# Kernel optimization log

Hardware: AMD Instinct MI355X
Metric: run time of the kernel (lower is better)

Reference implementation:

```python
import jax, jax.numpy as jnp
import numpy as np

K = 20
EPS = 1e-5


def _lrelu(x):
    return jax.nn.leaky_relu(x, 0.2)


def _bn(x, axes):
    # Training-mode batch norm with default affine (gamma=1, beta=0)
    m = jnp.mean(x, axis=axes, keepdims=True)
    v = jnp.var(x, axis=axes, keepdims=True)
    return (x - m) / jnp.sqrt(v + EPS)


def _get_graph_feature(x, k):
    # x: [B, C, N] -> [B, 2C, N, k]
    xx = jnp.sum(x * x, axis=1)                     # [B, N]
    inner = jnp.einsum('bcn,bcm->bnm', x, x)        # [B, N, N]
    pd = 2.0 * inner - xx[:, :, None] - xx[:, None, :]  # -||xi-xj||^2
    idx = jax.lax.top_k(pd, k)[1]                   # [B, N, k] nearest neighbors
    xt = jnp.transpose(x, (0, 2, 1))                # [B, N, C]
    feat = jax.vmap(lambda a, i: a[i])(xt, idx)     # [B, N, k, C] gathered neighbors
    center = jnp.broadcast_to(xt[:, :, None, :], feat.shape)
    out = jnp.concatenate([feat - center, center], axis=-1)  # [B, N, k, 2C]
    return jnp.transpose(out, (0, 3, 1, 2))


def _pconv(w, x):
    # 1x1 Conv2d, no bias: [O,C] x [B,C,N,k] -> [B,O,N,k]
    return jnp.einsum('oc,bcnk->bonk', w, x)


def _transform_net(x0, t_w1, t_w2, t_w3, t_fc1_w, t_fc2_w, t_fc2_b, t_fc3_w, t_fc3_b):
    h = _lrelu(_bn(_pconv(t_w1, x0), (0, 2, 3)))    # [B,64,N,k]
    h = _lrelu(_bn(_pconv(t_w2, h), (0, 2, 3)))     # [B,128,N,k]
    h = jnp.max(h, axis=-1)                         # [B,128,N]
    h = jnp.einsum('oc,bcn->bon', t_w3, h)          # [B,1024,N]
    h = _lrelu(_bn(h, (0, 2)))
    h = jnp.max(h, axis=-1)                         # [B,1024]
    h = _lrelu(_bn(h @ t_fc1_w.T, (0,)))            # [B,512]
    h = _lrelu(_bn(h @ t_fc2_w.T + t_fc2_b, (0,)))  # [B,256]
    h = h @ t_fc3_w.T + t_fc3_b                     # [B,9]
    h = h + jnp.eye(3, dtype=h.dtype).reshape(1, 9)
    return h.reshape(-1, 3, 3)


def setup_inputs() -> dict:
    key = jax.random.key(0)
    ks = jax.random.split(key, 16)
    s = 0.05
    B, N = 8, 1024
    return {
        'x': jax.random.normal(ks[0], (B, 3, N), jnp.float32),
        't_w1': jax.random.normal(ks[1], (64, 6), jnp.float32) * s,
        't_w2': jax.random.normal(ks[2], (128, 64), jnp.float32) * s,
        't_w3': jax.random.normal(ks[3], (1024, 128), jnp.float32) * s,
        't_fc1_w': jax.random.normal(ks[4], (512, 1024), jnp.float32) * s,
        't_fc2_w': jax.random.normal(ks[5], (256, 512), jnp.float32) * s,
        't_fc2_b': jnp.zeros((256,), jnp.float32),
        't_fc3_w': jax.random.normal(ks[6], (9, 256), jnp.float32) * s,
        't_fc3_b': jnp.zeros((9,), jnp.float32),
        'w1': jax.random.normal(ks[7], (64, 6), jnp.float32) * s,
        'w2': jax.random.normal(ks[8], (64, 128), jnp.float32) * s,
        'w3': jax.random.normal(ks[9], (128, 128), jnp.float32) * s,
        'w4': jax.random.normal(ks[10], (256, 256), jnp.float32) * s,
        'w6': jax.random.normal(ks[11], (1024, 512), jnp.float32) * s,
    }


def reference(x, t_w1, t_w2, t_w3, t_fc1_w, t_fc2_w, t_fc2_b, t_fc3_w, t_fc3_b,
              w1, w2, w3, w4, w6):
    # Input transform
    x0 = _get_graph_feature(x, K)                   # [B,6,N,k]
    T = _transform_net(x0, t_w1, t_w2, t_w3, t_fc1_w, t_fc2_w, t_fc2_b,
                       t_fc3_w, t_fc3_b)            # [B,3,3]
    x = jnp.einsum('bij,bjn->bin', T, x)            # [B,3,N]

    # EdgeConv stack
    g = _get_graph_feature(x, K)
    x1 = jnp.max(_lrelu(_bn(_pconv(w1, g), (0, 2, 3))), axis=-1)   # [B,64,N]
    g = _get_graph_feature(x1, K)
    x2 = jnp.max(_lrelu(_bn(_pconv(w2, g), (0, 2, 3))), axis=-1)   # [B,64,N]
    g = _get_graph_feature(x2, K)
    x3 = jnp.max(_lrelu(_bn(_pconv(w3, g), (0, 2, 3))), axis=-1)   # [B,128,N]
    g = _get_graph_feature(x3, K)
    x4 = jnp.max(_lrelu(_bn(_pconv(w4, g), (0, 2, 3))), axis=-1)   # [B,256,N]

    x_cat = jnp.concatenate([x1, x2, x3, x4], axis=1)              # [B,512,N]
    x_fea = x_cat  # adapt_layer_off: source unavailable, identity passthrough

    h = jnp.einsum('oc,bcn->bon', w6, x_fea)                       # [B,1024,N]
    h = _lrelu(_bn(h, (0, 2)))
    return jnp.max(h, axis=-1)                                     # [B,1024]
```

## Files before the change

kernel.cpp:

```cpp
#include <hip/hip_runtime.h>
#include <math.h>

#define BN_ 8
#define NN 1024
#define KK 20
#define EPSBN 1e-5f
#define FXSCALE 1048576.0f

typedef unsigned long long u64;

__device__ __forceinline__ float lrelu(float x){ return x > 0.f ? x : 0.2f*x; }

__device__ __forceinline__ unsigned fmap(float x){
  unsigned u = __float_as_uint(x);
  return (u & 0x80000000u) ? ~u : (u | 0x80000000u);
}
__device__ __forceinline__ float funmap(unsigned m){
  unsigned u = (m & 0x80000000u) ? (m & 0x7FFFFFFFu) : ~m;
  return __uint_as_float(u);
}

__device__ __forceinline__ int mbcnt64(u64 m){
  return __builtin_amdgcn_mbcnt_hi((unsigned)(m >> 32),
         __builtin_amdgcn_mbcnt_lo((unsigned)m, 0));
}

__device__ __forceinline__ void statadd(u64* SP, int O, int ch, int o, float s, float s2){
  atomicAdd(&SP[(size_t)ch*2*O + o],     (u64)(long long)llrintf(s  * FXSCALE));
  atomicAdd(&SP[(size_t)ch*2*O + O + o], (u64)(long long)llrintf(s2 * FXSCALE));
}

__global__ void k_transq(const float* __restrict__ src, long bs, int C,
                         float* __restrict__ xt, float* __restrict__ xx)
{
  int g = blockIdx.x*256 + threadIdx.x;
  if (g >= BN_*NN) return;
  int b = g >> 10, n = g & 1023;
  const float* s = src + (long)b*bs + n;
  float* d = xt + (long)g*C;
  float ss = 0.f;
  for (int c = 0; c < C; ++c){ float v = s[(long)c*NN]; d[c] = v; ss += v*v; }
  xx[g] = ss;
}

__global__ __launch_bounds__(256) void k_knn(
    const float* __restrict__ X, long bsX,
    const float* __restrict__ XT, const float* __restrict__ XX,
    int* __restrict__ IDX, int C)
{
  extern __shared__ float sm[];
  int tid = threadIdx.x;
  int wave = tid >> 6, lane = tid & 63;
  int b = blockIdx.x >> 7;
  int i0 = (blockIdx.x & 127) << 3;
  for (int t = tid; t < 8*C; t += 256){
    int rr = t / C, cc = t - rr*C;
    sm[t] = XT[((long)(b<<10) + i0 + rr)*C + cc];
  }
  __syncthreads();
  const float* xb = X + (long)b*bsX;
  float acc[2][16];
  #pragma unroll
  for (int r=0;r<2;r++)
    #pragma unroll
    for (int q=0;q<16;q++) acc[r][q]=0.f;
  const float* xi = sm + (wave*2)*C;
  for (int c = 0; c < C; ++c){
    const float4* xr4 = (const float4*)(xb + (long)c*NN);
    float4 xv4[4];
    #pragma unroll
    for (int q4=0;q4<4;q4++) xv4[q4] = xr4[q4*64 + lane];
    #pragma unroll
    for (int r=0;r<2;r++){
      float xiv = xi[r*C + c];
      #pragma unroll
      for (int q4=0;q4<4;q4++){
        acc[r][q4*4+0] = fmaf(xiv, xv4[q4].x, acc[r][q4*4+0]);
        acc[r][q4*4+1] = fmaf(xiv, xv4[q4].y, acc[r][q4*4+1]);
        acc[r][q4*4+2] = fmaf(xiv, xv4[q4].z, acc[r][q4*4+2]);
        acc[r][q4*4+3] = fmaf(xiv, xv4[q4].w, acc[r][q4*4+3]);
      }
    }
  }
  const float4* xx4 = (const float4*)(XX + (b<<10));
  float xxj[16];
  #pragma unroll
  for (int q4=0;q4<4;q4++){
    float4 t = xx4[q4*64 + lane];
    xxj[q4*4+0]=t.x; xxj[q4*4+1]=t.y; xxj[q4*4+2]=t.z; xxj[q4*4+3]=t.w;
  }
  const float* xxb = XX + (b<<10);
  int row0 = i0 + wave*2;
  #pragma unroll
  for (int r=0;r<2;r++){
    float xxi = xxb[row0 + r];
    #pragma unroll
    for (int q=0;q<16;q++) acc[r][q] = 2.f*acc[r][q] - xxi - xxj[q];
  }

  for (int r=0;r<2;r++){
    unsigned u[16];
    #pragma unroll
    for (int q=0;q<16;q++) u[q] = fmap(acc[r][q]);
    unsigned P = 0;
    for (int bit = 31; bit >= 0; --bit){
      unsigned cand = P | (1u << bit);
      int c = 0;
      #pragma unroll
      for (int q=0;q<16;q++) c += (int)__popcll(__ballot(u[q] >= cand));
      if (c >= KK) P = cand;
    }
    int nG = 0;
    #pragma unroll
    for (int q=0;q<16;q++) nG += (int)__popcll(__ballot(u[q] > P));
    int navail = KK - nG;
    int slot = 0;
    int outb = ((b<<10) + row0 + r)*KK;
    #pragma unroll
    for (int q=0;q<16;q++){
      u64 mg = __ballot(u[q] > P);
      u64 me = __ballot(u[q] == P);
      int cg = (int)__popcll(mg);
      int ce = (int)__popcll(me);
      int take_e = navail < ce ? navail : ce;
      int nval = ((q >> 2) << 8) + (lane << 2) + (q & 3);
      if (u[q] > P){
        IDX[outb + slot + mbcnt64(mg)] = nval;
      } else if (u[q] == P){
        int rk = mbcnt64(me);
        if (rk < take_e) IDX[outb + slot + cg + rk] = nval;
      }
      slot += cg + take_e;
      navail -= take_e;
    }
  }
}

__global__ void k_edgeconv3(const float* __restrict__ XT, const int* __restrict__ IDX,
                            const float* __restrict__ W, float* __restrict__ YMT,
                            u64* __restrict__ SP)
{
  __shared__ float nb[KK*3];
  __shared__ float ctr[3];
  __shared__ int is[KK];
  const int C = 3, O = 64;
  int tid = threadIdx.x;
  int bn = blockIdx.x;
  int b = bn >> 10;
  if (tid < KK) is[tid] = IDX[bn*KK + tid];
  __syncthreads();
  if (tid < 60){ int k = tid/3, c = tid - k*3; nb[tid] = XT[((long)(b<<10)+is[k])*C + c]; }
  if (tid < 3) ctr[tid] = XT[(long)bn*C + tid];
  __syncthreads();
  int o = tid;
  const float* wp = W + (long)o*2*C;
  float yc = 0.f;
  #pragma unroll
  for (int c = 0; c < 3; ++c) yc = fmaf(wp[C+c] - wp[c], ctr[c], yc);
  float acc[KK];
  #pragma unroll
  for (int k=0;k<KK;k++) acc[k] = yc;
  #pragma unroll
  for (int c = 0; c < 3; ++c){
    float wf = wp[c];
    #pragma unroll
    for (int k=0;k<KK;k++) acc[k] = fmaf(wf, nb[k*3+c], acc[k]);
  }
  float mx = -INFINITY, s = 0.f, s2 = 0.f;
  #pragma unroll
  for (int k=0;k<KK;k++){ float v = acc[k]; mx = fmaxf(mx, v); s += v; s2 = fmaf(v,v,s2); }
  YMT[(long)bn*O + o] = mx;
  statadd(SP, O, bn & 63, o, s, s2);
}

template<int C, int O>
__global__ __launch_bounds__(256) void k_gemm_ab(
    const float* __restrict__ XT, const float* __restrict__ WP,
    float* __restrict__ AB)
{
  constexpr int P = 16;
  constexpr int TWO = 2*O;
  constexpr int CO = (TWO + 255)/256;
  __shared__ __align__(16) float Xs[P][C];
  int tid = threadIdx.x;
  long bn0 = (long)blockIdx.x * P;
  for (int t = tid; t < P*C; t += 256) (&Xs[0][0])[t] = XT[bn0*C + t];
  __syncthreads();
  float acc[CO][P];
  #pragma unroll
  for (int j=0;j<CO;j++)
    #pragma unroll
    for (int r=0;r<P;r++) acc[j][r] = 0.f;
  for (int c4 = 0; c4 < C/4; ++c4){
    float4 w[CO];
    #pragma unroll
    for (int j=0;j<CO;j++){
      int o = tid + j*256;
      if (o < TWO) w[j] = *(const float4*)(WP + ((size_t)c4*TWO + o)*4);
    }
    #pragma unroll
    for (int r=0;r<P;r++){
      float4 xv = *(const float4*)(&Xs[r][c4*4]);
      #pragma unroll
      for (int j=0;j<CO;j++){
        acc[j][r] = fmaf(w[j].x, xv.x, acc[j][r]);
        acc[j][r] = fmaf(w[j].y, xv.y, acc[j][r]);
        acc[j][r] = fmaf(w[j].z, xv.z, acc[j][r]);
        acc[j][r] = fmaf(w[j].w, xv.w, acc[j][r]);
      }
    }
  }
  #pragma unroll
  for (int j=0;j<CO;j++){
    int o = tid + j*256;
    if (o < TWO)
      for (int r=0;r<P;r++) AB[(bn0 + r)*TWO + o] = acc[j][r];
  }
}

template<int O, int P>
__global__ __launch_bounds__(256) void k_egather(
    const float* __restrict__ AB, const int* __restrict__ IDX,
    float* __restrict__ YMT, u64* __restrict__ SP)
{
  constexpr int TWO = 2*O;
  constexpr int S = 256/O;
  constexpr int PS = P/S;
  __shared__ int is[P][KK];
  int tid = threadIdx.x;
  long bn0 = (long)blockIdx.x * P;
  long b10 = (bn0 >> 10) << 10;
  for (int t = tid; t < P*KK; t += 256) (&is[0][0])[t] = IDX[bn0*KK + t];
  __syncthreads();
  int strand = tid / O;
  int o = tid - strand*O;
  float s = 0.f, s2 = 0.f;
  #pragma unroll
  for (int ps = 0; ps < PS; ++ps){
    int p = strand*PS + ps;
    long bn = bn0 + p;
    float bv = AB[bn*TWO + O + o];
    float mx = -INFINITY;
    #pragma unroll
    for (int k = 0; k < KK; ++k){
      long row = b10 + is[p][k];
      float v = AB[row*TWO + o] + bv;
      mx = fmaxf(mx, v);
      s += v; s2 = fmaf(v,v,s2);
    }
    YMT[bn*O + o] = mx;
  }
  int ch = ((int)blockIdx.x * S + strand) & 63;
  statadd(SP, O, ch, o, s, s2);
}

__global__ void k_bnfin(const u64* __restrict__ SP, float* __restrict__ MV, int O, float cnt)
{
  int o = blockIdx.x*blockDim.x + threadIdx.x;
  if (o >= O) return;
  long long S = 0, S2 = 0;
  for (int ch = 0; ch < 64; ++ch){
    S  += (long long)SP[(size_t)ch*2*O + o];
    S2 += (long long)SP[(size_t)ch*2*O + O + o];
  }
  double m = (double)S / ((double)FXSCALE * (double)cnt);
  double ms2 = (double)S2 / ((double)FXSCALE * (double)cnt);
  double var = ms2 - m*m;
  MV[o] = (float)m;
  MV[O + o] = (float)(1.0 / sqrt(var + (double)EPSBN));
}

__global__ __launch_bounds__(64) void k_tconv2(
    const float* __restrict__ XT, const int* __restrict__ IDX,
    const float* __restrict__ W1, const float* __restrict__ MV1,
    const float* __restrict__ W2T, float* __restrict__ M2T, u64* __restrict__ SP)
{
  __shared__ float nb[KK*3];
  __shared__ float ctr[3];
  __shared__ __align__(16) float h1t[64*KK];
  __shared__ int is[KK];
  int tid = threadIdx.x;
  int bn = blockIdx.x;
  int b = bn >> 10;
  if (tid < KK) is[tid] = IDX[bn*KK + tid];
  __syncthreads();
  if (tid < 60){ int k = tid/3, c = tid - k*3; nb[tid] = XT[((long)(b<<10)+is[k])*3 + c]; }
  if (tid < 3) ctr[tid] = XT[(long)bn*3 + tid];
  __syncthreads();
  {
    const float* wp = W1 + tid*6;
    float w0=wp[0], w1=wp[1], w2=wp[2];
    float cterm = fmaf(wp[3]-w0, ctr[0], fmaf(wp[4]-w1, ctr[1], (wp[5]-w2)*ctr[2]));
    float m = MV1[tid], iv = MV1[64+tid];
    #pragma unroll
    for (int k=0;k<KK;k++){
      float y = cterm;
      y = fmaf(w0, nb[k*3],   y);
      y = fmaf(w1, nb[k*3+1], y);
      y = fmaf(w2, nb[k*3+2], y);
      h1t[tid*KK + k] = lrelu((y - m) * iv);
    }
  }
  __syncthreads();
  float acc[2][KK];
  #pragma unroll
  for (int j=0;j<2;j++)
    #pragma unroll
    for (int k=0;k<KK;k++) acc[j][k]=0.f;
  #pragma unroll 2
  for (int c=0;c<64;++c){
    float wv0 = W2T[c*128 + tid];
    float wv1 = W2T[c*128 + 64 + tid];
    const float4* hp = (const float4*)(h1t + c*KK);
    float hv[KK];
    #pragma unroll
    for (int q=0;q<5;q++){
      float4 v4 = hp[q];
      hv[q*4]=v4.x; hv[q*4+1]=v4.y; hv[q*4+2]=v4.z; hv[q*4+3]=v4.w;
    }
    #pragma unroll
    for (int k=0;k<KK;k++){
      acc[0][k] = fmaf(wv0, hv[k], acc[0][k]);
      acc[1][k] = fmaf(wv1, hv[k], acc[1][k]);
    }
  }
  int ch = bn & 63;
  #pragma unroll
  for (int j=0;j<2;j++){
    int o = tid + j*64;
    float mx=-INFINITY, s=0.f, s2=0.f;
    #pragma unroll
    for (int k=0;k<KK;k++){ float v = acc[j][k]; mx = fmaxf(mx, v); s += v; s2 = fmaf(v,v,s2); }
    M2T[(long)bn*128 + o] = mx;
    statadd(SP, 128, ch, o, s, s2);
  }
}

__global__ void k_apply_t(const float* __restrict__ SRC, const float* __restrict__ MV,
                          int O, float* __restrict__ DST, long dbs, int choff,
                          float* __restrict__ XTN, float* __restrict__ XXN)
{
  int bn = blockIdx.x*64 + threadIdx.x;
  if (bn >= BN_*NN) return;
  int b = bn >> 10, n = bn & 1023;
  const float4* src = (const float4*)(SRC + (long)bn*O);
  float4* xo = XTN ? (float4*)(XTN + (long)bn*O) : nullptr;
  float ss = 0.f;
  for (int o4 = 0; o4 < O/4; ++o4){
    float4 v = src[o4];
    float vv[4] = {v.x, v.y, v.z, v.w};
    float rr[4];
    #pragma unroll
    for (int u=0;u<4;u++){
      int o = o4*4+u;
      float t = lrelu((vv[u] - MV[o]) * MV[O+o]);
      rr[u] = t;
      ss = fmaf(t,t,ss);
      DST[(long)b*dbs + (long)(choff+o)*NN + n] = t;
    }
    if (xo) xo[o4] = make_float4(rr[0],rr[1],rr[2],rr[3]);
  }
  if (XXN) XXN[bn] = ss;
}

__global__ void k_wprep_t(const float* __restrict__ W, float* __restrict__ WT, int O, int C)
{
  int g = blockIdx.x*256+threadIdx.x;
  if (g >= O*C) return;
  int o = g / C, c = g - o*C;
  WT[(long)c*O + o] = W[g];
}

__global__ void k_wprep_q(const float* __restrict__ W, float* __restrict__ WQ, int C)
{
  int g = blockIdx.x*256+threadIdx.x;
  if (g >= 1024*C) return;
  int o = g / C, c = g - o*C;
  int j = o >> 8, t = o & 255;
  WQ[((size_t)c*256 + t)*4 + j] = W[g];
}

__global__ void k_wprep_e2(const float* __restrict__ W, float* __restrict__ WP, int O, int C)
{
  int g = blockIdx.x*256+threadIdx.x;
  if (g >= O*C) return;
  int o = g / C, c = g - o*C;
  float wf = W[(long)o*2*C + c];
  float wc = W[(long)o*2*C + C + c];
  size_t base = ((size_t)(c>>2)*(2*O))*4 + (c&3);
  WP[base + (size_t)o*4]       = wf;
  WP[base + (size_t)(O+o)*4]   = wc - wf;
}

__global__ __launch_bounds__(256, 1) void k_gemm_sm(
    const float* __restrict__ WQ, const float* __restrict__ X,
    long bsX, int C, unsigned* __restrict__ MX, u64* __restrict__ SP)
{
  int tid = threadIdx.x;
  int bt = blockIdx.x;
  int b = bt >> 6;
  int n0 = (bt & 63) << 4;
  const float* xrow = X + (long)b*bsX + n0;
  float acc[4][16];
  #pragma unroll
  for (int j=0;j<4;j++)
    #pragma unroll
    for (int i=0;i<16;i++) acc[j][i]=0.f;
  const float4* wq = (const float4*)WQ;

  auto loadX = [&](int cc, float4* dst){
    const float4* xc = (const float4*)(xrow + (size_t)cc*NN);
    dst[0]=xc[0]; dst[1]=xc[1]; dst[2]=xc[2]; dst[3]=xc[3];
  };
  auto gemm_step = [&](const float4* xq, float4 wv){
    float4 xa = xq[0], xb2 = xq[1], xe = xq[2], xf = xq[3];
    float wj[4] = {wv.x, wv.y, wv.z, wv.w};
    #pragma unroll
    for (int j=0;j<4;j++){
      float ww = wj[j];
      acc[j][0]=fmaf(ww,xa.x,acc[j][0]);  acc[j][1]=fmaf(ww,xa.y,acc[j][1]);
      acc[j][2]=fmaf(ww,xa.z,acc[j][2]);  acc[j][3]=fmaf(ww,xa.w,acc[j][3]);
      acc[j][4]=fmaf(ww,xb2.x,acc[j][4]);  acc[j][5]=fmaf(ww,xb2.y,acc[j][5]);
      acc[j][6]=fmaf(ww,xb2.z,acc[j][6]);  acc[j][7]=fmaf(ww,xb2.w,acc[j][7]);
      acc[j][8]=fmaf(ww,xe.x,acc[j][8]);  acc[j][9]=fmaf(ww,xe.y,acc[j][9]);
      acc[j][10]=fmaf(ww,xe.z,acc[j][10]); acc[j][11]=fmaf(ww,xe.w,acc[j][11]);
      acc[j][12]=fmaf(ww,xf.x,acc[j][12]); acc[j][13]=fmaf(ww,xf.y,acc[j][13]);
      acc[j][14]=fmaf(ww,xf.z,acc[j][14]); acc[j][15]=fmaf(ww,xf.w,acc[j][15]);
    }
  };

  float4 xc0[4], xc1[4], xn0[4], xn1[4];
  loadX(0, xc0); loadX(1, xc1);
  float4 w0 = wq[tid];
  float4 w1 = wq[256 + tid];
  for (int c = 0; c < C-2; c += 2){
    loadX(c+2, xn0); loadX(c+3, xn1);
    float4 p0 = wq[(size_t)(c+2)*256 + tid];
    float4 p1 = wq[(size_t)(c+3)*256 + tid];
    gemm_step(xc0, w0);
    gemm_step(xc1, w1);
    #pragma unroll
    for (int i=0;i<4;i++){ xc0[i]=xn0[i]; xc1[i]=xn1[i]; }
    w0 = p0; w1 = p1;
  }
  gemm_step(xc0, w0);
  gemm_step(xc1, w1);

  int ch = bt & 63;
  #pragma unroll
  for (int j=0;j<4;j++){
    int o = tid + j*256;
    float mx=-INFINITY, s=0.f, s2=0.f;
    #pragma unroll
    for (int i=0;i<16;i++){ float v=acc[j][i]; mx=fmaxf(mx,v); s+=v; s2=fmaf(v,v,s2); }
    atomicMax(&MX[(b<<10) + o], fmap(mx));
    statadd(SP, 1024, ch, o, s, s2);
  }
}

__global__ void k_finmax(const unsigned* __restrict__ MX, const float* __restrict__ MV,
                         float* __restrict__ OUT)
{
  int g = blockIdx.x*256+threadIdx.x;
  if (g >= BN_*1024) return;
  int o = g & 1023;
  OUT[g] = lrelu((funmap(MX[g]) - MV[o]) * MV[1024+o]);
}

__global__ __launch_bounds__(256) void k_fcbn(
    const float* __restrict__ A, const float* __restrict__ W,
    const float* __restrict__ bias, int C, int F, float* __restrict__ Z)
{
  int wv = threadIdx.x >> 6, lane = threadIdx.x & 63;
  int f = blockIdx.x*4 + wv;
  if (f >= F) return;
  const float* w = W + (long)f*C;
  float acc[8];
  #pragma unroll
  for (int b=0;b<8;b++) acc[b]=0.f;
  for (int c = lane; c < C; c += 64){
    float wvv = w[c];
    #pragma unroll
    for (int b=0;b<8;b++) acc[b] = fmaf(wvv, A[b*C + c], acc[b]);
  }
  #pragma unroll
  for (int b=0;b<8;b++){
    #pragma unroll
    for (int off=32; off>0; off>>=1) acc[b] += __shfl_xor(acc[b], off);
  }
  float bs = bias ? bias[f] : 0.f;
  float m = 0.f;
  #pragma unroll
  for (int b=0;b<8;b++){ acc[b] += bs; m += acc[b]; }
  m *= 0.125f;
  float var = 0.f;
  #pragma unroll
  for (int b=0;b<8;b++){ float d = acc[b]-m; var = fmaf(d,d,var); }
  var *= 0.125f;
  float is = rsqrtf(var + EPSBN);
  if (lane < 8) Z[lane*F + f] = lrelu((acc[lane]-m)*is);
}

__global__ __launch_bounds__(256) void k_fc3w(
    const float* __restrict__ A, const float* __restrict__ W,
    const float* __restrict__ bias, float* __restrict__ T9)
{
  int g = blockIdx.x*4 + (threadIdx.x >> 6);
  int lane = threadIdx.x & 63;
  if (g >= 72) return;
  int b = g / 9, j = g - b*9;
  const float* a = A + b*256;
  const float* w = W + j*256;
  float s = 0.f;
  for (int c = lane; c < 256; c += 64) s = fmaf(a[c], w[c], s);
  #pragma unroll
  for (int off=32; off>0; off>>=1) s += __shfl_xor(s, off);
  if (lane == 0){
    s += bias[j];
    if (j==0 || j==4 || j==8) s += 1.f;
    T9[g] = s;
  }
}

__global__ void k_tapply(const float* __restrict__ Xin, const float* __restrict__ T9,
                         float* __restrict__ Xtr)
{
  int g = blockIdx.x*256+threadIdx.x;
  if (g >= BN_*3*NN) return;
  int n = g & 1023;
  int i = (g >> 10) % 3;
  int b = g / (3*NN);
  const float* t = T9 + b*9 + i*3;
  const float* xb = Xin + (long)b*3*NN + n;
  Xtr[g] = fmaf(t[0], xb[0], fmaf(t[1], xb[NN], t[2]*xb[2*NN]));
}

extern "C" void kernel_launch(void* const* d_in, const int* in_sizes, int n_in,
                              void* d_out, int out_size, void* d_ws, size_t ws_size,
                              hipStream_t stream)
{
  (void)in_sizes; (void)n_in; (void)out_size;
  const float* x     = (const float*)d_in[0];
  const float* tw1   = (const float*)d_in[1];
  const float* tw2   = (const float*)d_in[2];
  const float* tw3   = (const float*)d_in[3];
  const float* tfc1w = (const float*)d_in[4];
  const float* tfc2w = (const float*)d_in[5];
  const float* tfc2b = (const float*)d_in[6];
  const float* tfc3w = (const float*)d_in[7];
  const float* tfc3b = (const float*)d_in[8];
  const float* w1    = (const float*)d_in[9];
  const float* w2    = (const float*)d_in[10];
  const float* w3    = (const float*)d_in[11];
  const float* w4    = (const float*)d_in[12];
  const float* w6    = (const float*)d_in[13];
  float* out = (float*)d_out;

  char* ws = (char*)d_ws;
  size_t off = 0;
  auto alloc = [&](size_t bytes) -> void* {
    off = (off + 255) & ~(size_t)255;
    void* p = ws + off;
    off += bytes;
    return p;
  };
  auto spb = [](int O){ return (size_t)64*2*O*8; };

  float*    xt   = (float*)alloc((size_t)BN_*NN*128*4);
  float*    xx   = (float*)alloc((size_t)BN_*NN*4);
  int*      idx  = (int*)  alloc((size_t)BN_*NN*KK*4);
  float*    ymt  = (float*)alloc((size_t)BN_*NN*256*4);
  float*    ab   = (float*)alloc((size_t)BN_*NN*512*4);
  float*    xcat = (float*)alloc((size_t)BN_*512*NN*4);
  float*    xtr  = (float*)alloc((size_t)BN_*3*NN*4);
  float*    m2   = (float*)alloc((size_t)BN_*128*NN*4);
  size_t zoff0 = (off + 255) & ~(size_t)255;
  u64*      sp_e1 = (u64*)alloc(spb(64));
  u64*      sp_tc = (u64*)alloc(spb(128));
  u64*      sp_g1 = (u64*)alloc(spb(1024));
  u64*      sp_L1 = (u64*)alloc(spb(64));
  u64*      sp_L2 = (u64*)alloc(spb(64));
  u64*      sp_L3 = (u64*)alloc(spb(128));
  u64*      sp_L4 = (u64*)alloc(spb(256));
  u64*      sp_g2 = (u64*)alloc(spb(1024));
  unsigned* mxu1  = (unsigned*)alloc((size_t)BN_*1024*4);
  unsigned* mxu2  = (unsigned*)alloc((size_t)BN_*1024*4);
  size_t ztotal = off - zoff0;
  float*    mv1  = (float*)alloc(2*64*4);
  float*    mv2  = (float*)alloc(2*128*4);
  float*    mv3  = (float*)alloc(2*1024*4);
  float*    mvL  = (float*)alloc(2*256*4);
  float*    mv6  = (float*)alloc(2*1024*4);
  float*    vbuf = (float*)alloc((size_t)BN_*1024*4);
  float*    z1   = (float*)alloc((size_t)BN_*512*4);
  float*    z2   = (float*)alloc((size_t)BN_*256*4);
  float*    T9   = (float*)alloc(72*4);
  float*    wt3q = (float*)alloc((size_t)128*1024*4);
  float*    w6q  = (float*)alloc((size_t)512*1024*4);
  float*    wt2t = (float*)alloc((size_t)64*128*4);
  float*    w2p  = (float*)alloc((size_t)64*128*4);
  float*    w3p  = (float*)alloc((size_t)64*256*4);
  float*    w4p  = (float*)alloc((size_t)128*512*4);
  if (off > ws_size) return;

  float* m2t = ymt;

  const float CNTK = 8.f*1024.f*20.f;
  const float CNTN = 8.f*1024.f;

  hipMemsetAsync((char*)ws + zoff0, 0, ztotal, stream);

  k_wprep_t<<<(128*64+255)/256, 256, 0, stream>>>(tw2, wt2t, 128, 64);
  k_wprep_q<<<(1024*128)/256, 256, 0, stream>>>(tw3, wt3q, 128);
  k_wprep_q<<<(1024*512)/256, 256, 0, stream>>>(w6, w6q, 512);
  k_wprep_e2<<<(64*64+255)/256, 256, 0, stream>>>(w2, w2p, 64, 64);
  k_wprep_e2<<<(128*64+255)/256, 256, 0, stream>>>(w3, w3p, 128, 64);
  k_wprep_e2<<<(256*128+255)/256, 256, 0, stream>>>(w4, w4p, 256, 128);

  k_transq<<<32, 256, 0, stream>>>(x, 3L*NN, 3, xt, xx);
  k_knn<<<1024, 256, 8*3*4, stream>>>(x, 3L*NN, xt, xx, idx, 3);
  k_edgeconv3<<<BN_*NN, 64, 0, stream>>>(xt, idx, tw1, ymt, sp_e1);
  k_bnfin<<<1, 64, 0, stream>>>(sp_e1, mv1, 64, CNTK);
  k_tconv2<<<BN_*NN, 64, 0, stream>>>(xt, idx, tw1, mv1, wt2t, m2t, sp_tc);
  k_bnfin<<<2, 64, 0, stream>>>(sp_tc, mv2, 128, CNTK);
  k_apply_t<<<128, 64, 0, stream>>>(m2t, mv2, 128, m2, 128L*NN, 0, nullptr, nullptr);
  k_gemm_sm<<<BN_*64, 256, 0, stream>>>(wt3q, m2, 128L*NN, 128, mxu1, sp_g1);
  k_bnfin<<<16, 64, 0, stream>>>(sp_g1, mv3, 1024, CNTN);
  k_finmax<<<32, 256, 0, stream>>>(mxu1, mv3, vbuf);
  k_fcbn<<<128, 256, 0, stream>>>(vbuf, tfc1w, nullptr, 1024, 512, z1);
  k_fcbn<<<64, 256, 0, stream>>>(z1, tfc2w, tfc2b, 512, 256, z2);
  k_fc3w<<<18, 256, 0, stream>>>(z2, tfc3w, tfc3b, T9);
  k_tapply<<<(BN_*3*NN)/256, 256, 0, stream>>>(x, T9, xtr);

  k_transq<<<32, 256, 0, stream>>>(xtr, 3L*NN, 3, xt, xx);
  k_knn<<<1024, 256, 8*3*4, stream>>>(xtr, 3L*NN, xt, xx, idx, 3);
  k_edgeconv3<<<BN_*NN, 64, 0, stream>>>(xt, idx, w1, ymt, sp_L1);
  k_bnfin<<<1, 64, 0, stream>>>(sp_L1, mvL, 64, CNTK);
  k_apply_t<<<128, 64, 0, stream>>>(ymt, mvL, 64, xcat, 512L*NN, 0, xt, xx);
  k_knn<<<1024, 256, 8*64*4, stream>>>(xcat, 512L*NN, xt, xx, idx, 64);
  k_gemm_ab<64,64><<<512, 256, 0, stream>>>(xt, w2p, ab);
  k_egather<64,16><<<512, 256, 0, stream>>>(ab, idx, ymt, sp_L2);
  k_bnfin<<<1, 64, 0, stream>>>(sp_L2, mvL, 64, CNTK);
  k_apply_t<<<128, 64, 0, stream>>>(ymt, mvL, 64, xcat, 512L*NN, 64, xt, xx);
  k_knn<<<1024, 256, 8*64*4, stream>>>(xcat + 64L*NN, 512L*NN, xt, xx, idx, 64);
  k_gemm_ab<64,128><<<512, 256, 0, stream>>>(xt, w3p, ab);
  k_egather<128,16><<<512, 256, 0, stream>>>(ab, idx, ymt, sp_L3);
  k_bnfin<<<2, 64, 0, stream>>>(sp_L3, mvL, 128, CNTK);
  k_apply_t<<<128, 64, 0, stream>>>(ymt, mvL, 128, xcat, 512L*NN, 128, xt, xx);
  k_knn<<<1024, 256, 8*128*4, stream>>>(xcat + 128L*NN, 512L*NN, xt, xx, idx, 128);
  k_gemm_ab<128,256><<<512, 256, 0, stream>>>(xt, w4p, ab);
  k_egather<256,16><<<512, 256, 0, stream>>>(ab, idx, ymt, sp_L4);
  k_bnfin<<<4, 64, 0, stream>>>(sp_L4, mvL, 256, CNTK);
  k_apply_t<<<128, 64, 0, stream>>>(ymt, mvL, 256, xcat, 512L*NN, 256, nullptr, nullptr);

  k_gemm_sm<<<BN_*64, 256, 0, stream>>>(w6q, xcat, 512L*NN, 512, mxu2, sp_g2);
  k_bnfin<<<16, 64, 0, stream>>>(sp_g2, mv6, 1024, CNTN);
  k_finmax<<<32, 256, 0, stream>>>(mxu2, mv6, out);
}
```

Measured before the change: 861.4 us.

## Run final 512→1024 conv GEMM on bf16 MFMA with fused max/BN stats

Replaces the fp32 SIMT GEMM for the final w6 layer with a bf16 MFMA 16x16x32 kernel. The weights are pre-swizzled into fragment layout, and k_apply_t additionally writes a bf16 point-major copy of the concatenated features via LDS staging. The goal is to cut the FMA-bound cost of the largest GEMM, at the price of bf16 rounding in the BN statistics and max, plus extra writes in apply. The k_gemm_sm prefetch double-buffer is also simplified, which affects the transform-net GEMM.

```diff
diff --git a/kernel.cpp b/kernel.cpp
--- a/kernel.cpp
+++ b/kernel.cpp
@@ -8,6 +8,9 @@
 #define FXSCALE 1048576.0f
 
 typedef unsigned long long u64;
+typedef unsigned short ushort_t;
+typedef __attribute__((ext_vector_type(8))) short short8v;
+typedef __attribute__((ext_vector_type(4))) float f32x4;
 
 __device__ __forceinline__ float lrelu(float x){ return x > 0.f ? x : 0.2f*x; }
 
@@ -18,6 +21,11 @@
 __device__ __forceinline__ float funmap(unsigned m){
   unsigned u = (m & 0x80000000u) ? (m & 0x7FFFFFFFu) : ~m;
   return __uint_as_float(u);
+}
+__device__ __forceinline__ ushort_t f2b(float f){
+  unsigned u = __float_as_uint(f);
+  unsigned r = (u + 0x7FFFu + ((u >> 16) & 1u)) >> 16;
+  return (ushort_t)r;
 }
 
 __device__ __forceinline__ int mbcnt64(u64 m){
@@ -338,10 +346,11 @@
 
 __global__ void k_apply_t(const float* __restrict__ SRC, const float* __restrict__ MV,
                           int O, float* __restrict__ DST, long dbs, int choff,
-                          float* __restrict__ XTN, float* __restrict__ XXN)
-{
+                          float* __restrict__ XTN, float* __restrict__ XXN,
+                          ushort_t* __restrict__ XB)
+{
+  extern __shared__ ushort_t lb[];
   int bn = blockIdx.x*64 + threadIdx.x;
-  if (bn >= BN_*NN) return;
   int b = bn >> 10, n = bn & 1023;
   const float4* src = (const float4*)(SRC + (long)bn*O);
   float4* xo = XTN ? (float4*)(XTN + (long)bn*O) : nullptr;
@@ -357,10 +366,19 @@
       rr[u] = t;
       ss = fmaf(t,t,ss);
       DST[(long)b*dbs + (long)(choff+o)*NN + n] = t;
+      if (XB) lb[threadIdx.x*O + o] = f2b(t);
     }
     if (xo) xo[o4] = make_float4(rr[0],rr[1],rr[2],rr[3]);
   }
   if (XXN) XXN[bn] = ss;
+  if (XB){
+    __syncthreads();
+    long bn0 = (long)blockIdx.x*64;
+    for (int r = 0; r < 64; ++r){
+      for (int t2 = threadIdx.x; t2 < O; t2 += 64)
+        XB[(bn0 + r)*512 + choff + t2] = lb[r*O + t2];
+    }
+  }
 }
 
 __global__ void k_wprep_t(const float* __restrict__ W, float* __restrict__ WT, int O, int C)
@@ -378,6 +396,17 @@
   int o = g / C, c = g - o*C;
   int j = o >> 8, t = o & 255;
   WQ[((size_t)c*256 + t)*4 + j] = W[g];
+}
+
+__global__ void k_wprep_mf(const float* __restrict__ W, ushort_t* __restrict__ WB)
+{
+  int g = blockIdx.x*256+threadIdx.x;
+  if (g >= 1024*512) return;
+  int o = g >> 9, c = g & 511;
+  int ks = c >> 5, kk = c & 31;
+  int l = (kk >> 3)*16 + (o & 15);
+  int e = kk & 7;
+  WB[(((size_t)(o >> 4)*16 + ks)*64 + l)*8 + e] = f2b(W[g]);
 }
 
 __global__ void k_wprep_e2(const float* __restrict__ W, float* __restrict__ WP, int O, int C)
@@ -408,12 +437,9 @@
     for (int i=0;i<16;i++) acc[j][i]=0.f;
   const float4* wq = (const float4*)WQ;
 
-  auto loadX = [&](int cc, float4* dst){
+  auto gemm_step = [&](int cc, float4 wv){
     const float4* xc = (const float4*)(xrow + (size_t)cc*NN);
-    dst[0]=xc[0]; dst[1]=xc[1]; dst[2]=xc[2]; dst[3]=xc[3];
-  };
-  auto gemm_step = [&](const float4* xq, float4 wv){
-    float4 xa = xq[0], xb2 = xq[1], xe = xq[2], xf = xq[3];
+    float4 xa = xc[0], xb2 = xc[1], xe = xc[2], xf = xc[3];
     float wj[4] = {wv.x, wv.y, wv.z, wv.w};
     #pragma unroll
     for (int j=0;j<4;j++){
@@ -429,22 +455,17 @@
     }
   };
 
-  float4 xc0[4], xc1[4], xn0[4], xn1[4];
-  loadX(0, xc0); loadX(1, xc1);
   float4 w0 = wq[tid];
   float4 w1 = wq[256 + tid];
   for (int c = 0; c < C-2; c += 2){
-    loadX(c+2, xn0); loadX(c+3, xn1);
     float4 p0 = wq[(size_t)(c+2)*256 + tid];
     float4 p1 = wq[(size_t)(c+3)*256 + tid];
-    gemm_step(xc0, w0);
-    gemm_step(xc1, w1);
-    #pragma unroll
-    for (int i=0;i<4;i++){ xc0[i]=xn0[i]; xc1[i]=xn1[i]; }
+    gemm_step(c,   w0);
+    gemm_step(c+1, w1);
     w0 = p0; w1 = p1;
   }
-  gemm_step(xc0, w0);
-  gemm_step(xc1, w1);
+  gemm_step(C-2, w0);
+  gemm_step(C-1, w1);
 
   int ch = bt & 63;
   #pragma unroll
@@ -454,6 +475,53 @@
     #pragma unroll
     for (int i=0;i<16;i++){ float v=acc[j][i]; mx=fmaxf(mx,v); s+=v; s2=fmaf(v,v,s2); }
     atomicMax(&MX[(b<<10) + o], fmap(mx));
+    statadd(SP, 1024, ch, o, s, s2);
+  }
+}
+
+__global__ __launch_bounds__(256) void k_gemm_mfma(
+    const ushort_t* __restrict__ WB, const ushort_t* __restrict__ XB,
+    unsigned* __restrict__ MX, u64* __restrict__ SP)
+{
+  int tid = threadIdx.x;
+  int w = tid >> 6, lane = tid & 63;
+  int b = blockIdx.x >> 4;
+  int ob = blockIdx.x & 15;
+  int otile = ob*4 + w;
+  int o0 = otile << 4;
+  short8v wfrag[16];
+  const short8v* wp = (const short8v*)WB;
+  #pragma unroll
+  for (int ks=0; ks<16; ++ks)
+    wfrag[ks] = wp[((size_t)otile*16 + ks)*64 + lane];
+
+  float mx = -INFINITY, s = 0.f, s2 = 0.f;
+  int nbase = blockIdx.y*256;
+  for (int nt = 0; nt < 16; ++nt){
+    int n0 = nbase + nt*16;
+    const short8v* xp = (const short8v*)(XB + ((size_t)(b<<10) + n0 + (lane & 15))*512 + (lane >> 4)*8);
+    f32x4 acc = {0.f, 0.f, 0.f, 0.f};
+    #pragma unroll
+    for (int ks=0; ks<16; ++ks){
+      short8v a = xp[ks*4];
+      acc = __builtin_amdgcn_mfma_f32_16x16x32_bf16(a, wfrag[ks], acc, 0, 0, 0);
+    }
+    #pragma unroll
+    for (int reg=0; reg<4; ++reg){
+      float v = acc[reg];
+      mx = fmaxf(mx, v); s += v; s2 = fmaf(v, v, s2);
+    }
+  }
+  #pragma unroll
+  for (int off=16; off<=32; off<<=1){
+    mx = fmaxf(mx, __shfl_xor(mx, off));
+    s += __shfl_xor(s, off);
+    s2 += __shfl_xor(s2, off);
+  }
+  if (lane < 16){
+    int o = o0 + lane;
+    atomicMax(&MX[(b<<10) + o], fmap(mx));
+    int ch = ((blockIdx.x << 2) + w + (blockIdx.y << 4)) & 63;
     statadd(SP, 1024, ch, o, s, s2);
   }
 }
@@ -574,6 +642,8 @@
   float*    xcat = (float*)alloc((size_t)BN_*512*NN*4);
   float*    xtr  = (float*)alloc((size_t)BN_*3*NN*4);
   float*    m2   = (float*)alloc((size_t)BN_*128*NN*4);
+  ushort_t* xb16 = (ushort_t*)alloc((size_t)BN_*NN*512*2);
+  ushort_t* wb16 = (ushort_t*)alloc((size_t)1024*512*2);
   size_t zoff0 = (off + 255) & ~(size_t)255;
   u64*      sp_e1 = (u64*)alloc(spb(64));
   u64*      sp_tc = (u64*)alloc(spb(128));
@@ -596,7 +666,6 @@
   float*    z2   = (float*)alloc((size_t)BN_*256*4);
   float*    T9   = (float*)alloc(72*4);
   float*    wt3q = (float*)alloc((size_t)128*1024*4);
-  float*    w6q  = (float*)alloc((size_t)512*1024*4);
   float*    wt2t = (float*)alloc((size_t)64*128*4);
   float*    w2p  = (float*)alloc((size_t)64*128*4);
   float*    w3p  = (float*)alloc((size_t)64*256*4);
@@ -612,7 +681,7 @@
 
   k_wprep_t<<<(128*64+255)/256, 256, 0, stream>>>(tw2, wt2t, 128, 64);
   k_wprep_q<<<(1024*128)/256, 256, 0, stream>>>(tw3, wt3q, 128);
-  k_wprep_q<<<(1024*512)/256, 256, 0, stream>>>(w6, w6q, 512);
+  k_wprep_mf<<<(1024*512)/256, 256, 0, stream>>>(w6, wb16);
   k_wprep_e2<<<(64*64+255)/256, 256, 0, stream>>>(w2, w2p, 64, 64);
   k_wprep_e2<<<(128*64+255)/256, 256, 0, stream>>>(w3, w3p, 128, 64);
   k_wprep_e2<<<(256*128+255)/256, 256, 0, stream>>>(w4, w4p, 256, 128);
@@ -623,7 +692,7 @@
   k_bnfin<<<1, 64, 0, stream>>>(sp_e1, mv1, 64, CNTK);
   k_tconv2<<<BN_*NN, 64, 0, stream>>>(xt, idx, tw1, mv1, wt2t, m2t, sp_tc);
   k_bnfin<<<2, 64, 0, stream>>>(sp_tc, mv2, 128, CNTK);
-  k_apply_t<<<128, 64, 0, stream>>>(m2t, mv2, 128, m2, 128L*NN, 0, nullptr, nullptr);
+  k_apply_t<<<128, 64, 0, stream>>>(m2t, mv2, 128, m2, 128L*NN, 0, nullptr, nullptr, nullptr);
   k_gemm_sm<<<BN_*64, 256, 0, stream>>>(wt3q, m2, 128L*NN, 128, mxu1, sp_g1);
   k_bnfin<<<16, 64, 0, stream>>>(sp_g1, mv3, 1024, CNTN);
   k_finmax<<<32, 256, 0, stream>>>(mxu1, mv3, vbuf);
@@ -636,24 +705,24 @@
   k_knn<<<1024, 256, 8*3*4, stream>>>(xtr, 3L*NN, xt, xx, idx, 3);
   k_edgeconv3<<<BN_*NN, 64, 0, stream>>>(xt, idx, w1, ymt, sp_L1);
   k_bnfin<<<1, 64, 0, stream>>>(sp_L1, mvL, 64, CNTK);
-  k_apply_t<<<128, 64, 0, stream>>>(ymt, mvL, 64, xcat, 512L*NN, 0, xt, xx);
+  k_apply_t<<<128, 64, 64*64*2, stream>>>(ymt, mvL, 64, xcat, 512L*NN, 0, xt, xx, xb16);
   k_knn<<<1024, 256, 8*64*4, stream>>>(xcat, 512L*NN, xt, xx, idx, 64);
   k_gemm_ab<64,64><<<512, 256, 0, stream>>>(xt, w2p, ab);
   k_egather<64,16><<<512, 256, 0, stream>>>(ab, idx, ymt, sp_L2);
   k_bnfin<<<1, 64, 0, stream>>>(sp_L2, mvL, 64, CNTK);
-  k_apply_t<<<128, 64, 0, stream>>>(ymt, mvL, 64, xcat, 512L*NN, 64, xt, xx);
+  k_apply_t<<<128, 64, 64*64*2, stream>>>(ymt, mvL, 64, xcat, 512L*NN, 64, xt, xx, xb16);
   k_knn<<<1024, 256, 8*64*4, stream>>>(xcat + 64L*NN, 512L*NN, xt, xx, idx, 64);
   k_gemm_ab<64,128><<<512, 256, 0, stream>>>(xt, w3p, ab);
   k_egather<128,16><<<512, 256, 0, stream>>>(ab, idx, ymt, sp_L3);
   k_bnfin<<<2, 64, 0, stream>>>(sp_L3, mvL, 128, CNTK);
-  k_apply_t<<<128, 64, 0, stream>>>(ymt, mvL, 128, xcat, 512L*NN, 128, xt, xx);
+  k_apply_t<<<128, 64, 64*128*2, stream>>>(ymt, mvL, 128, xcat, 512L*NN, 128, xt, xx, xb16);
   k_knn<<<1024, 256, 8*128*4, stream>>>(xcat + 128L*NN, 512L*NN, xt, xx, idx, 128);
   k_gemm_ab<128,256><<<512, 256, 0, stream>>>(xt, w4p, ab);
   k_egather<256,16><<<512, 256, 0, stream>>>(ab, idx, ymt, sp_L4);
   k_bnfin<<<4, 64, 0, stream>>>(sp_L4, mvL, 256, CNTK);
-  k_apply_t<<<128, 64, 0, stream>>>(ymt, mvL, 256, xcat, 512L*NN, 256, nullptr, nullptr);
-
-  k_gemm_sm<<<BN_*64, 256, 0, stream>>>(w6q, xcat, 512L*NN, 512, mxu2, sp_g2);
+  k_apply_t<<<128, 64, 64*256*2, stream>>>(ymt, mvL, 256, xcat, 512L*NN, 256, nullptr, nullptr, xb16);
+
+  k_gemm_mfma<<<dim3(BN_*16, 4), 256, 0, stream>>>(wb16, xb16, mxu2, sp_g2);
   k_bnfin<<<16, 64, 0, stream>>>(sp_g2, mv6, 1024, CNTN);
   k_finmax<<<32, 256, 0, stream>>>(mxu2, mv6, out);
 }
```

Measured after the change: 860.0 us. No clear change (-0.2%).
